# Kernel optimization log

Hardware: AMD Instinct MI355X
Metric: run time of the kernel (lower is better)

## Reference

```python
import jax, jax.numpy as jnp
import numpy as np

N_NODES = 50000
N_EDGES = 600000
IN_FEATS = 128
N_HIDDEN = 128
N_CLASSES = 64


def setup_inputs() -> dict:
    key = jax.random.key(0)
    ks = jax.random.split(key, 10)
    x = jax.random.normal(ks[0], (N_NODES, IN_FEATS), dtype=jnp.float32)
    w = jax.random.uniform(ks[1], (N_EDGES,), dtype=jnp.float32)
    src = jax.random.randint(ks[2], (N_EDGES,), 0, N_NODES, dtype=jnp.int32)
    dst = jax.random.randint(ks[3], (N_EDGES,), 0, N_NODES, dtype=jnp.int32)
    W1 = jax.random.normal(ks[4], (IN_FEATS, N_HIDDEN), dtype=jnp.float32) * 0.05
    b1 = jnp.zeros((N_HIDDEN,), dtype=jnp.float32)
    W2 = jax.random.normal(ks[5], (N_HIDDEN, N_HIDDEN), dtype=jnp.float32) * 0.05
    b2 = jnp.zeros((N_HIDDEN,), dtype=jnp.float32)
    W3 = jax.random.normal(ks[6], (N_HIDDEN, N_CLASSES), dtype=jnp.float32) * 0.05
    b3 = jnp.zeros((N_CLASSES,), dtype=jnp.float32)
    return {"x": x, "w": w, "src": src, "dst": dst,
            "W1": W1, "b1": b1, "W2": W2, "b2": b2, "W3": W3, "b3": b3}


def _graph_conv(h, Wl, bl, w, src, dst, n_nodes):
    # dense linear transform
    h = h @ Wl + bl  # [N, d_out]
    # u_mul_e: gather source features, scale by edge weight
    m = h[src] * w[:, None]  # [E, d_out]
    # sum aggregation into destination nodes
    return jax.ops.segment_sum(m, dst, num_segments=n_nodes)  # [N, d_out]


def reference(x, w, src, dst, W1, b1, W2, b2, W3, b3):
    n = x.shape[0]
    h = jax.nn.relu(_graph_conv(x, W1, b1, w, src, dst, n))
    h = jax.nn.relu(_graph_conv(h, W2, b2, w, src, dst, n))
    return _graph_conv(h, W3, b3, w, src, dst, n)
```

## Files before the change

kernel.cpp:

```cpp
#include <hip/hip_runtime.h>
#include <hip/hip_fp16.h>


typedef __attribute__((ext_vector_type(8))) short short8;
typedef __attribute__((ext_vector_type(4))) float float4v;

constexpr int CAP  = 48;
constexpr int CPAD = 16;

__device__ inline unsigned bf16_rne(float f) {
    unsigned u = __float_as_uint(f);
    return (u + 0x7FFF + ((u >> 16) & 1)) >> 16;
}
__device__ inline float bf_lo(unsigned t) { return __uint_as_float(t << 16); }
__device__ inline float bf_hi(unsigned t) { return __uint_as_float(t & 0xFFFF0000u); }

__device__ inline unsigned pack_rec(int s, float wv) {
    return ((unsigned)__half_as_ushort(__float2half(wv)) << 16) | (unsigned)s;
}
__device__ inline float rec_w(unsigned r) {
    return __half2float(__ushort_as_half((unsigned short)(r >> 16)));
}
__device__ inline int rec_src(unsigned r) { return (int)(r & 0xFFFFu); }

__device__ inline void wprep_one(const float* __restrict__ Wm, int M, int tt,
                                 unsigned short* __restrict__ WfH,
                                 unsigned short* __restrict__ WfL) {
    const int FT = M / 16;
    int lane = tt & 63;
    int ft   = (tt >> 6) % FT;
    int ks   = tt / (64 * FT);
    int n     = ft * 16 + (lane & 15);
    int kbase = ks * 32 + (lane >> 4) * 8;
    #pragma unroll
    for (int j = 0; j < 8; j++) {
        float wv = Wm[(size_t)(kbase + j) * M + n];
        unsigned hb = bf16_rne(wv);
        float wh = __uint_as_float(hb << 16);
        unsigned lb = bf16_rne(wv - wh);
        WfH[(size_t)tt * 8 + j] = (unsigned short)hb;
        WfL[(size_t)tt * 8 + j] = (unsigned short)lb;
    }
}

__global__ void prep_kernel(const float* __restrict__ W1, const float* __restrict__ W2,
                            const float* __restrict__ W3,
                            unsigned short* WfH1, unsigned short* WfL1,
                            unsigned short* WfH2, unsigned short* WfL2,
                            unsigned short* WfH3, unsigned short* WfL3,
                            int* __restrict__ countsP, int N) {
    int t = blockIdx.x * blockDim.x + threadIdx.x;
    if (t < 2048)       wprep_one(W1, 128, t,        WfH1, WfL1);
    else if (t < 4096)  wprep_one(W2, 128, t - 2048, WfH2, WfL2);
    else if (t < 5120)  wprep_one(W3,  64, t - 4096, WfH3, WfL3);
    for (int i = t; i < N; i += gridDim.x * blockDim.x) countsP[i * CPAD] = 0;
}

__global__ __launch_bounds__(256) void l1_fused(
        const float* __restrict__ H,
        const unsigned short* __restrict__ WfH, const unsigned short* __restrict__ WfL,
        const float* __restrict__ bias, unsigned short* __restrict__ T,
        const int* __restrict__ src, const int* __restrict__ dst,
        const float* __restrict__ w, int* __restrict__ countsP,
        unsigned* __restrict__ erec, int N, int E, int SB) {
    const int K  = 128;
    const int KP = K + 4;
    const int M  = 128;
    const int FT = M / 16;
    __shared__ float Hs[64 * KP];

    if ((int)blockIdx.x < SB) {
        int e = (blockIdx.x * 256 + threadIdx.x) * 4;
        if (e + 3 < E) {
            int4   d4 = *(const int4*)(dst + e);
            int4   s4 = *(const int4*)(src + e);
            float4 w4 = *(const float4*)(w + e);
            unsigned r0 = pack_rec(s4.x, w4.x);
            unsigned r1 = pack_rec(s4.y, w4.y);
            unsigned r2 = pack_rec(s4.z, w4.z);
            unsigned r3 = pack_rec(s4.w, w4.w);
            int p0 = atomicAdd(&countsP[d4.x * CPAD], 1);
            int p1 = atomicAdd(&countsP[d4.y * CPAD], 1);
            int p2 = atomicAdd(&countsP[d4.z * CPAD], 1);
            int p3 = atomicAdd(&countsP[d4.w * CPAD], 1);
            if (p0 < CAP) erec[(size_t)d4.x * CAP + p0] = r0;
            if (p1 < CAP) erec[(size_t)d4.y * CAP + p1] = r1;
            if (p2 < CAP) erec[(size_t)d4.z * CAP + p2] = r2;
            if (p3 < CAP) erec[(size_t)d4.w * CAP + p3] = r3;
        } else {
            for (; e < E; e++) {
                int d = dst[e];
                unsigned r = pack_rec(src[e], w[e]);
                int p = atomicAdd(&countsP[d * CPAD], 1);
                if (p < CAP) erec[(size_t)d * CAP + p] = r;
            }
        }
        return;
    }

    const int node0 = (blockIdx.x - SB) * 64;
    for (int i = threadIdx.x; i < 64 * (K / 4); i += 256) {
        int r = i / (K / 4), c = i % (K / 4);
        int node = node0 + r;
        float4 hv = {0, 0, 0, 0};
        if (node < N) hv = ((const float4*)(H + (size_t)node * K))[c];
        *(float4*)(Hs + r * KP + c * 4) = hv;
    }
    __syncthreads();

    const int wave = threadIdx.x >> 6;
    const int lane = threadIdx.x & 63;
    const int row  = lane & 15;
    const int ksub = (lane >> 4) * 8;
    const float* hrow = Hs + (wave * 16 + row) * KP;

    float4v acc[FT];
    #pragma unroll
    for (int ft = 0; ft < FT; ft++) acc[ft] = (float4v){0.f, 0.f, 0.f, 0.f};

    #pragma unroll
    for (int ks = 0; ks < 4; ks++) {
        const float* ap = hrow + ks * 32 + ksub;
        float4 a0 = *(const float4*)(ap);
        float4 a1 = *(const float4*)(ap + 4);
        float av[8] = {a0.x, a0.y, a0.z, a0.w, a1.x, a1.y, a1.z, a1.w};
        short8 ah, al;
        #pragma unroll
        for (int j = 0; j < 8; j++) {
            unsigned hb = bf16_rne(av[j]);
            float fh = __uint_as_float(hb << 16);
            ah[j] = (short)hb;
            al[j] = (short)bf16_rne(av[j] - fh);
        }
        #pragma unroll
        for (int ft = 0; ft < FT; ft++) {
            short8 bh = *(const short8*)(WfH + ((size_t)(ks * FT + ft) * 64 + lane) * 8);
            short8 bl = *(const short8*)(WfL + ((size_t)(ks * FT + ft) * 64 + lane) * 8);
            acc[ft] = __builtin_amdgcn_mfma_f32_16x16x32_bf16(ah, bh, acc[ft], 0, 0, 0);
            acc[ft] = __builtin_amdgcn_mfma_f32_16x16x32_bf16(al, bh, acc[ft], 0, 0, 0);
            acc[ft] = __builtin_amdgcn_mfma_f32_16x16x32_bf16(ah, bl, acc[ft], 0, 0, 0);
        }
    }

    const int col   = lane & 15;
    const int rbase = (lane >> 4) * 4;
    #pragma unroll
    for (int ft = 0; ft < FT; ft++) {
        int feat = ft * 16 + col;
        float bv = bias[feat];
        #pragma unroll
        for (int r = 0; r < 4; r++) {
            int node = node0 + wave * 16 + rbase + r;
            if (node < N)
                T[(size_t)node * M + feat] = (unsigned short)bf16_rne(acc[ft][r] + bv);
        }
    }
}

template <int M>
__global__ __launch_bounds__(256) void gemm_bf_kernel(const unsigned short* __restrict__ Hb,
                                                      const unsigned short* __restrict__ WfH,
                                                      const unsigned short* __restrict__ WfL,
                                                      const float* __restrict__ bias,
                                                      unsigned short* __restrict__ T, int N) {
    const int FT = M / 16;
    const int wave = threadIdx.x >> 6;
    const int lane = threadIdx.x & 63;
    const int row  = lane & 15;
    const int ksub = (lane >> 4) * 8;
    const int node0 = blockIdx.x * 64;
    int nodeA = node0 + wave * 16 + row;
    const unsigned short* hp = Hb + (size_t)(nodeA < N ? nodeA : N - 1) * 128;

    float4v acc[FT];
    #pragma unroll
    for (int ft = 0; ft < FT; ft++) acc[ft] = (float4v){0.f, 0.f, 0.f, 0.f};

    #pragma unroll
    for (int ks = 0; ks < 4; ks++) {
        short8 ah = *(const short8*)(hp + ks * 32 + ksub);
        #pragma unroll
        for (int ft = 0; ft < FT; ft++) {
            short8 bh = *(const short8*)(WfH + ((size_t)(ks * FT + ft) * 64 + lane) * 8);
            short8 bl = *(const short8*)(WfL + ((size_t)(ks * FT + ft) * 64 + lane) * 8);
            acc[ft] = __builtin_amdgcn_mfma_f32_16x16x32_bf16(ah, bh, acc[ft], 0, 0, 0);
            acc[ft] = __builtin_amdgcn_mfma_f32_16x16x32_bf16(ah, bl, acc[ft], 0, 0, 0);
        }
    }

    const int col   = lane & 15;
    const int rbase = (lane >> 4) * 4;
    #pragma unroll
    for (int ft = 0; ft < FT; ft++) {
        int feat = ft * 16 + col;
        float bv = bias[feat];
        #pragma unroll
        for (int r = 0; r < 4; r++) {
            int node = node0 + wave * 16 + rbase + r;
            if (node < N)
                T[(size_t)node * M + feat] = (unsigned short)bf16_rne(acc[ft][r] + bv);
        }
    }
}

__global__ void agg128_bf(const unsigned short* __restrict__ Tin,
                          const int* __restrict__ countsP,
                          const unsigned* __restrict__ erec,
                          unsigned short* __restrict__ Hb, int N) {
    const int wid  = threadIdx.x >> 6;
    const int lane = threadIdx.x & 63;
    const int v0 = blockIdx.x * 8 + wid * 2;
    if (v0 >= N) return;
    const int v1 = (v0 + 1 < N) ? v0 + 1 : v0;
    const int q  = lane >> 4;
    const int fo = (lane & 15) * 8;
    const unsigned* eb0 = erec + (size_t)v0 * CAP;
    const unsigned* eb1 = erec + (size_t)v1 * CAP;

    int rx0[4], rx1[4]; float wv0[4], wv1[4];
    #pragma unroll
    for (int u = 0; u < 4; u++) {
        unsigned r0 = eb0[u * 4 + q];
        unsigned r1 = eb1[u * 4 + q];
        rx0[u] = rec_src(r0); wv0[u] = rec_w(r0);
        rx1[u] = rec_src(r1); wv1[u] = rec_w(r1);
    }
    const int c0 = min(countsP[v0 * CPAD], CAP);
    const int c1 = min(countsP[v1 * CPAD], CAP);
    const int cm = max(c0, c1);

    float A0[8] = {0, 0, 0, 0, 0, 0, 0, 0};
    float A1[8] = {0, 0, 0, 0, 0, 0, 0, 0};
    for (int i = 0; i < cm; i += 16) {
        #pragma unroll
        for (int u = 0; u < 4; u++) {
            int idx = i + u * 4 + q;
            if (idx < c0) {
                uint4 t = *(const uint4*)(Tin + (size_t)rx0[u] * 128 + fo);
                float wu = wv0[u];
                A0[0] = fmaf(wu, bf_lo(t.x), A0[0]); A0[1] = fmaf(wu, bf_hi(t.x), A0[1]);
                A0[2] = fmaf(wu, bf_lo(t.y), A0[2]); A0[3] = fmaf(wu, bf_hi(t.y), A0[3]);
                A0[4] = fmaf(wu, bf_lo(t.z), A0[4]); A0[5] = fmaf(wu, bf_hi(t.z), A0[5]);
                A0[6] = fmaf(wu, bf_lo(t.w), A0[6]); A0[7] = fmaf(wu, bf_hi(t.w), A0[7]);
            }
            if (idx < c1) {
                uint4 t = *(const uint4*)(Tin + (size_t)rx1[u] * 128 + fo);
                float wu = wv1[u];
                A1[0] = fmaf(wu, bf_lo(t.x), A1[0]); A1[1] = fmaf(wu, bf_hi(t.x), A1[1]);
                A1[2] = fmaf(wu, bf_lo(t.y), A1[2]); A1[3] = fmaf(wu, bf_hi(t.y), A1[3]);
                A1[4] = fmaf(wu, bf_lo(t.z), A1[4]); A1[5] = fmaf(wu, bf_hi(t.z), A1[5]);
                A1[6] = fmaf(wu, bf_lo(t.w), A1[6]); A1[7] = fmaf(wu, bf_hi(t.w), A1[7]);
            }
        }
        if (i + 16 < cm) {
            #pragma unroll
            for (int u = 0; u < 4; u++) {
                unsigned r0 = eb0[i + 16 + u * 4 + q];
                unsigned r1 = eb1[i + 16 + u * 4 + q];
                rx0[u] = rec_src(r0); wv0[u] = rec_w(r0);
                rx1[u] = rec_src(r1); wv1[u] = rec_w(r1);
            }
        }
    }
    #pragma unroll
    for (int j = 0; j < 8; j++) {
        A0[j] += __shfl_xor(A0[j], 32); A1[j] += __shfl_xor(A1[j], 32);
        A0[j] += __shfl_xor(A0[j], 16); A1[j] += __shfl_xor(A1[j], 16);
    }
    if (lane < 16) {
        short8 o;
        #pragma unroll
        for (int j = 0; j < 8; j++) o[j] = (short)bf16_rne(fmaxf(A0[j], 0.f));
        *(short8*)(Hb + (size_t)v0 * 128 + fo) = o;
    } else if (lane < 32 && v1 != v0) {
        short8 o;
        #pragma unroll
        for (int j = 0; j < 8; j++) o[j] = (short)bf16_rne(fmaxf(A1[j], 0.f));
        *(short8*)(Hb + (size_t)v1 * 128 + fo) = o;
    }
}

__global__ void agg_final_v4(const unsigned short* __restrict__ Tin,
                             const int* __restrict__ countsP,
                             const unsigned* __restrict__ erec,
                             float* __restrict__ OUT, int N) {
    const int wid  = threadIdx.x >> 6;
    const int lane = threadIdx.x & 63;
    const int v0 = blockIdx.x * 8 + wid * 2;
    if (v0 >= N) return;
    const int v1 = (v0 + 1 < N) ? v0 + 1 : v0;
    const int o8 = lane >> 3;
    const int fo = (lane & 7) * 8;
    const unsigned* eb0 = erec + (size_t)v0 * CAP;
    const unsigned* eb1 = erec + (size_t)v1 * CAP;

    int rx0[2], rx1[2]; float wv0[2], wv1[2];
    #pragma unroll
    for (int u = 0; u < 2; u++) {
        unsigned r0 = eb0[u * 8 + o8];
        unsigned r1 = eb1[u * 8 + o8];
        rx0[u] = rec_src(r0); wv0[u] = rec_w(r0);
        rx1[u] = rec_src(r1); wv1[u] = rec_w(r1);
    }
    const int c0 = min(countsP[v0 * CPAD], CAP);
    const int c1 = min(countsP[v1 * CPAD], CAP);
    const int cm = max(c0, c1);

    float A0[8] = {0, 0, 0, 0, 0, 0, 0, 0};
    float A1[8] = {0, 0, 0, 0, 0, 0, 0, 0};
    for (int i = 0; i < cm; i += 16) {
        #pragma unroll
        for (int u = 0; u < 2; u++) {
            int idx = i + u * 8 + o8;
            if (idx < c0) {
                uint4 t = *(const uint4*)(Tin + (size_t)rx0[u] * 64 + fo);
                float wu = wv0[u];
                A0[0] = fmaf(wu, bf_lo(t.x), A0[0]); A0[1] = fmaf(wu, bf_hi(t.x), A0[1]);
                A0[2] = fmaf(wu, bf_lo(t.y), A0[2]); A0[3] = fmaf(wu, bf_hi(t.y), A0[3]);
                A0[4] = fmaf(wu, bf_lo(t.z), A0[4]); A0[5] = fmaf(wu, bf_hi(t.z), A0[5]);
                A0[6] = fmaf(wu, bf_lo(t.w), A0[6]); A0[7] = fmaf(wu, bf_hi(t.w), A0[7]);
            }
            if (idx < c1) {
                uint4 t = *(const uint4*)(Tin + (size_t)rx1[u] * 64 + fo);
                float wu = wv1[u];
                A1[0] = fmaf(wu, bf_lo(t.x), A1[0]); A1[1] = fmaf(wu, bf_hi(t.x), A1[1]);
                A1[2] = fmaf(wu, bf_lo(t.y), A1[2]); A1[3] = fmaf(wu, bf_hi(t.y), A1[3]);
                A1[4] = fmaf(wu, bf_lo(t.z), A1[4]); A1[5] = fmaf(wu, bf_hi(t.z), A1[5]);
                A1[6] = fmaf(wu, bf_lo(t.w), A1[6]); A1[7] = fmaf(wu, bf_hi(t.w), A1[7]);
            }
        }
        if (i + 16 < cm) {
            #pragma unroll
            for (int u = 0; u < 2; u++) {
                unsigned r0 = eb0[i + 16 + u * 8 + o8];
                unsigned r1 = eb1[i + 16 + u * 8 + o8];
                rx0[u] = rec_src(r0); wv0[u] = rec_w(r0);
                rx1[u] = rec_src(r1); wv1[u] = rec_w(r1);
            }
        }
    }
    #pragma unroll
    for (int j = 0; j < 8; j++) {
        A0[j] += __shfl_xor(A0[j], 32); A1[j] += __shfl_xor(A1[j], 32);
        A0[j] += __shfl_xor(A0[j], 16); A1[j] += __shfl_xor(A1[j], 16);
        A0[j] += __shfl_xor(A0[j], 8);  A1[j] += __shfl_xor(A1[j], 8);
    }
    if (lane < 8) {
        float4 o0 = {A0[0], A0[1], A0[2], A0[3]};
        float4 o1 = {A0[4], A0[5], A0[6], A0[7]};
        float* op = OUT + (size_t)v0 * 64 + fo;
        *(float4*)(op)     = o0;
        *(float4*)(op + 4) = o1;
    } else if (lane < 16 && v1 != v0) {
        float4 o0 = {A1[0], A1[1], A1[2], A1[3]};
        float4 o1 = {A1[4], A1[5], A1[6], A1[7]};
        float* op = OUT + (size_t)v1 * 64 + fo;
        *(float4*)(op)     = o0;
        *(float4*)(op + 4) = o1;
    }
}

extern "C" void kernel_launch(void* const* d_in, const int* in_sizes, int n_in,
                              void* d_out, int out_size, void* d_ws, size_t ws_size,
                              hipStream_t stream) {
    const float* x   = (const float*)d_in[0];
    const float* w   = (const float*)d_in[1];
    const int*   src = (const int*)d_in[2];
    const int*   dst = (const int*)d_in[3];
    const float* W1  = (const float*)d_in[4];
    const float* b1  = (const float*)d_in[5];
    const float* W2  = (const float*)d_in[6];
    const float* b2  = (const float*)d_in[7];
    const float* W3  = (const float*)d_in[8];
    const float* b3  = (const float*)d_in[9];
    const int N = in_sizes[0] / 128;
    const int E = in_sizes[1];

    unsigned short* Tbf  = (unsigned short*)d_ws;
    unsigned short* Hbf  = Tbf + (size_t)N * 128;
    unsigned* erec = (unsigned*)(Hbf + (size_t)N * 128);
    int*  countsP  = (int*)(erec + (size_t)N * CAP);
    size_t coff = (size_t)((char*)(countsP + (size_t)N * CPAD) - (char*)d_ws);
    coff = (coff + 15) & ~(size_t)15;
    unsigned short* WfH1 = (unsigned short*)((char*)d_ws + coff);
    unsigned short* WfL1 = WfH1 + 128 * 128;
    unsigned short* WfH2 = WfL1 + 128 * 128;
    unsigned short* WfL2 = WfH2 + 128 * 128;
    unsigned short* WfH3 = WfL2 + 128 * 128;
    unsigned short* WfL3 = WfH3 + 128 * 64;

    const int GB = (N + 63) / 64;
    const int SB = (E / 4 + 255) / 256;
    const int AB = (N + 7) / 8;

    prep_kernel<<<96, 256, 0, stream>>>(W1, W2, W3, WfH1, WfL1, WfH2, WfL2,
                                        WfH3, WfL3, countsP, N);
    l1_fused<<<SB + GB, 256, 0, stream>>>(x, WfH1, WfL1, b1, Tbf,
                                          src, dst, w, countsP, erec, N, E, SB);
    agg128_bf<<<AB, 256, 0, stream>>>(Tbf, countsP, erec, Hbf, N);
    gemm_bf_kernel<128><<<GB, 256, 0, stream>>>(Hbf, WfH2, WfL2, b2, Tbf, N);
    agg128_bf<<<AB, 256, 0, stream>>>(Tbf, countsP, erec, Hbf, N);
    gemm_bf_kernel<64><<<GB, 256, 0, stream>>>(Hbf, WfH3, WfL3, b3, Tbf, N);
    agg_final_v4<<<AB, 256, 0, stream>>>(Tbf, countsP, erec, (float*)d_out, N);
}
```

Before: 240.7 us.

## Fuse neighbor aggregation with next-layer GEMM through shared memory

Merges each aggregation kernel with the following dense transform. A 512-thread block aggregates 16 nodes into shared memory, then each wave computes one 16-column output tile with MFMA. This removes the intermediate H round trip through global memory and two kernel launches, and ping-pongs between two T buffers. It also shrinks the layer-1 GEMM tile to 32 nodes per block with column-split waves to get more blocks. The cost is lower MFMA reuse per block and a block-wide barrier between the gather and GEMM phases; in the 64-column layer half the waves sit idle during the GEMM.

```diff
diff --git a/kernel.cpp b/kernel.cpp
--- a/kernel.cpp
+++ b/kernel.cpp
@@ -65,9 +65,7 @@
         unsigned* __restrict__ erec, int N, int E, int SB) {
     const int K  = 128;
     const int KP = K + 4;
-    const int M  = 128;
-    const int FT = M / 16;
-    __shared__ float Hs[64 * KP];
+    __shared__ float Hs[32 * KP];
 
     if ((int)blockIdx.x < SB) {
         int e = (blockIdx.x * 256 + threadIdx.x) * 4;
@@ -98,9 +96,9 @@
         return;
     }
 
-    const int node0 = (blockIdx.x - SB) * 64;
-    for (int i = threadIdx.x; i < 64 * (K / 4); i += 256) {
-        int r = i / (K / 4), c = i % (K / 4);
+    const int node0 = (blockIdx.x - SB) * 32;
+    for (int i = threadIdx.x; i < 32 * (K / 4); i += 256) {
+        int r = i >> 5, c = i & 31;
         int node = node0 + r;
         float4 hv = {0, 0, 0, 0};
         if (node < N) hv = ((const float4*)(H + (size_t)node * K))[c];
@@ -112,11 +110,13 @@
     const int lane = threadIdx.x & 63;
     const int row  = lane & 15;
     const int ksub = (lane >> 4) * 8;
-    const float* hrow = Hs + (wave * 16 + row) * KP;
-
-    float4v acc[FT];
-    #pragma unroll
-    for (int ft = 0; ft < FT; ft++) acc[ft] = (float4v){0.f, 0.f, 0.f, 0.f};
+    const int rbase16 = (wave >> 1) * 16;
+    const int ftbase  = (wave & 1) * 4;
+    const float* hrow = Hs + (rbase16 + row) * KP;
+
+    float4v acc[4];
+    #pragma unroll
+    for (int ft = 0; ft < 4; ft++) acc[ft] = (float4v){0.f, 0.f, 0.f, 0.f};
 
     #pragma unroll
     for (int ks = 0; ks < 4; ks++) {
@@ -133,9 +133,10 @@
             al[j] = (short)bf16_rne(av[j] - fh);
         }
         #pragma unroll
-        for (int ft = 0; ft < FT; ft++) {
-            short8 bh = *(const short8*)(WfH + ((size_t)(ks * FT + ft) * 64 + lane) * 8);
-            short8 bl = *(const short8*)(WfL + ((size_t)(ks * FT + ft) * 64 + lane) * 8);
+        for (int ft = 0; ft < 4; ft++) {
+            int ftg = ftbase + ft;
+            short8 bh = *(const short8*)(WfH + ((size_t)(ks * 8 + ftg) * 64 + lane) * 8);
+            short8 bl = *(const short8*)(WfL + ((size_t)(ks * 8 + ftg) * 64 + lane) * 8);
             acc[ft] = __builtin_amdgcn_mfma_f32_16x16x32_bf16(ah, bh, acc[ft], 0, 0, 0);
             acc[ft] = __builtin_amdgcn_mfma_f32_16x16x32_bf16(al, bh, acc[ft], 0, 0, 0);
             acc[ft] = __builtin_amdgcn_mfma_f32_16x16x32_bf16(ah, bl, acc[ft], 0, 0, 0);
@@ -145,77 +146,38 @@
     const int col   = lane & 15;
     const int rbase = (lane >> 4) * 4;
     #pragma unroll
-    for (int ft = 0; ft < FT; ft++) {
-        int feat = ft * 16 + col;
+    for (int ft = 0; ft < 4; ft++) {
+        int feat = (ftbase + ft) * 16 + col;
         float bv = bias[feat];
         #pragma unroll
         for (int r = 0; r < 4; r++) {
-            int node = node0 + wave * 16 + rbase + r;
+            int node = node0 + rbase16 + rbase + r;
             if (node < N)
-                T[(size_t)node * M + feat] = (unsigned short)bf16_rne(acc[ft][r] + bv);
-        }
-    }
-}
-
-template <int M>
-__global__ __launch_bounds__(256) void gemm_bf_kernel(const unsigned short* __restrict__ Hb,
-                                                      const unsigned short* __restrict__ WfH,
-                                                      const unsigned short* __restrict__ WfL,
-                                                      const float* __restrict__ bias,
-                                                      unsigned short* __restrict__ T, int N) {
-    const int FT = M / 16;
-    const int wave = threadIdx.x >> 6;
-    const int lane = threadIdx.x & 63;
-    const int row  = lane & 15;
-    const int ksub = (lane >> 4) * 8;
-    const int node0 = blockIdx.x * 64;
-    int nodeA = node0 + wave * 16 + row;
-    const unsigned short* hp = Hb + (size_t)(nodeA < N ? nodeA : N - 1) * 128;
-
-    float4v acc[FT];
-    #pragma unroll
-    for (int ft = 0; ft < FT; ft++) acc[ft] = (float4v){0.f, 0.f, 0.f, 0.f};
-
-    #pragma unroll
-    for (int ks = 0; ks < 4; ks++) {
-        short8 ah = *(const short8*)(hp + ks * 32 + ksub);
-        #pragma unroll
-        for (int ft = 0; ft < FT; ft++) {
-            short8 bh = *(const short8*)(WfH + ((size_t)(ks * FT + ft) * 64 + lane) * 8);
-            short8 bl = *(const short8*)(WfL + ((size_t)(ks * FT + ft) * 64 + lane) * 8);
-            acc[ft] = __builtin_amdgcn_mfma_f32_16x16x32_bf16(ah, bh, acc[ft], 0, 0, 0);
-            acc[ft] = __builtin_amdgcn_mfma_f32_16x16x32_bf16(ah, bl, acc[ft], 0, 0, 0);
-        }
-    }
-
-    const int col   = lane & 15;
-    const int rbase = (lane >> 4) * 4;
-    #pragma unroll
-    for (int ft = 0; ft < FT; ft++) {
-        int feat = ft * 16 + col;
-        float bv = bias[feat];
-        #pragma unroll
-        for (int r = 0; r < 4; r++) {
-            int node = node0 + wave * 16 + rbase + r;
-            if (node < N)
-                T[(size_t)node * M + feat] = (unsigned short)bf16_rne(acc[ft][r] + bv);
-        }
-    }
-}
-
-__global__ void agg128_bf(const unsigned short* __restrict__ Tin,
-                          const int* __restrict__ countsP,
-                          const unsigned* __restrict__ erec,
-                          unsigned short* __restrict__ Hb, int N) {
+                T[(size_t)node * 128 + feat] = (unsigned short)bf16_rne(acc[ft][r] + bv);
+        }
+    }
+}
+
+template <int MOUT>
+__global__ __launch_bounds__(512) void agg_gemm(
+        const unsigned short* __restrict__ Tin,
+        const int* __restrict__ countsP,
+        const unsigned* __restrict__ erec,
+        const unsigned short* __restrict__ WfH, const unsigned short* __restrict__ WfL,
+        const float* __restrict__ bias,
+        unsigned short* __restrict__ T, int N) {
+    constexpr int FT = MOUT / 16;
     const int wid  = threadIdx.x >> 6;
     const int lane = threadIdx.x & 63;
-    const int v0 = blockIdx.x * 8 + wid * 2;
-    if (v0 >= N) return;
-    const int v1 = (v0 + 1 < N) ? v0 + 1 : v0;
+    __shared__ unsigned short Hsm[16][136];
+
+    int v0 = blockIdx.x * 16 + wid * 2;
+    int v0c = (v0 < N) ? v0 : N - 1;
+    int v1c = (v0 + 1 < N) ? v0 + 1 : N - 1;
     const int q  = lane >> 4;
     const int fo = (lane & 15) * 8;
-    const unsigned* eb0 = erec + (size_t)v0 * CAP;
-    const unsigned* eb1 = erec + (size_t)v1 * CAP;
+    const unsigned* eb0 = erec + (size_t)v0c * CAP;
+    const unsigned* eb1 = erec + (size_t)v1c * CAP;
 
     int rx0[4], rx1[4]; float wv0[4], wv1[4];
     #pragma unroll
@@ -225,8 +187,8 @@
         rx0[u] = rec_src(r0); wv0[u] = rec_w(r0);
         rx1[u] = rec_src(r1); wv1[u] = rec_w(r1);
     }
-    const int c0 = min(countsP[v0 * CPAD], CAP);
-    const int c1 = min(countsP[v1 * CPAD], CAP);
+    const int c0 = min(countsP[v0c * CPAD], CAP);
+    const int c1 = min(countsP[v1c * CPAD], CAP);
     const int cm = max(c0, c1);
 
     float A0[8] = {0, 0, 0, 0, 0, 0, 0, 0};
@@ -271,12 +233,38 @@
         short8 o;
         #pragma unroll
         for (int j = 0; j < 8; j++) o[j] = (short)bf16_rne(fmaxf(A0[j], 0.f));
-        *(short8*)(Hb + (size_t)v0 * 128 + fo) = o;
-    } else if (lane < 32 && v1 != v0) {
+        *(short8*)&Hsm[wid * 2][lane * 8] = o;
+    } else if (lane < 32) {
         short8 o;
         #pragma unroll
         for (int j = 0; j < 8; j++) o[j] = (short)bf16_rne(fmaxf(A1[j], 0.f));
-        *(short8*)(Hb + (size_t)v1 * 128 + fo) = o;
+        *(short8*)&Hsm[wid * 2 + 1][(lane & 15) * 8] = o;
+    }
+    __syncthreads();
+
+    if (FT == 8 || wid < FT) {
+        const int ftg  = wid;
+        const int row  = lane & 15;
+        const int ksub = (lane >> 4) * 8;
+        float4v acc = (float4v){0.f, 0.f, 0.f, 0.f};
+        #pragma unroll
+        for (int ks = 0; ks < 4; ks++) {
+            short8 ah = *(const short8*)&Hsm[row][ks * 32 + ksub];
+            short8 bh = *(const short8*)(WfH + ((size_t)(ks * FT + ftg) * 64 + lane) * 8);
+            short8 bl = *(const short8*)(WfL + ((size_t)(ks * FT + ftg) * 64 + lane) * 8);
+            acc = __builtin_amdgcn_mfma_f32_16x16x32_bf16(ah, bh, acc, 0, 0, 0);
+            acc = __builtin_amdgcn_mfma_f32_16x16x32_bf16(ah, bl, acc, 0, 0, 0);
+        }
+        const int col   = lane & 15;
+        const int rbase = (lane >> 4) * 4;
+        const int feat  = ftg * 16 + col;
+        const float bv  = bias[feat];
+        #pragma unroll
+        for (int r = 0; r < 4; r++) {
+            int node = blockIdx.x * 16 + rbase + r;
+            if (node < N)
+                T[(size_t)node * MOUT + feat] = (unsigned short)bf16_rne(acc[r] + bv);
+        }
     }
 }
 
@@ -376,9 +364,9 @@
     const int N = in_sizes[0] / 128;
     const int E = in_sizes[1];
 
-    unsigned short* Tbf  = (unsigned short*)d_ws;
-    unsigned short* Hbf  = Tbf + (size_t)N * 128;
-    unsigned* erec = (unsigned*)(Hbf + (size_t)N * 128);
+    unsigned short* Ta   = (unsigned short*)d_ws;
+    unsigned short* Tb   = Ta + (size_t)N * 128;
+    unsigned* erec = (unsigned*)(Tb + (size_t)N * 128);
     int*  countsP  = (int*)(erec + (size_t)N * CAP);
     size_t coff = (size_t)((char*)(countsP + (size_t)N * CPAD) - (char*)d_ws);
     coff = (coff + 15) & ~(size_t)15;
@@ -389,17 +377,16 @@
     unsigned short* WfH3 = WfL2 + 128 * 128;
     unsigned short* WfL3 = WfH3 + 128 * 64;
 
-    const int GB = (N + 63) / 64;
-    const int SB = (E / 4 + 255) / 256;
-    const int AB = (N + 7) / 8;
+    const int GB  = (N + 31) / 32;
+    const int SB  = (E / 4 + 255) / 256;
+    const int AGB = (N + 15) / 16;
+    const int AB  = (N + 7) / 8;
 
     prep_kernel<<<96, 256, 0, stream>>>(W1, W2, W3, WfH1, WfL1, WfH2, WfL2,
                                         WfH3, WfL3, countsP, N);
-    l1_fused<<<SB + GB, 256, 0, stream>>>(x, WfH1, WfL1, b1, Tbf,
+    l1_fused<<<SB + GB, 256, 0, stream>>>(x, WfH1, WfL1, b1, Ta,
                                           src, dst, w, countsP, erec, N, E, SB);
-    agg128_bf<<<AB, 256, 0, stream>>>(Tbf, countsP, erec, Hbf, N);
-    gemm_bf_kernel<128><<<GB, 256, 0, stream>>>(Hbf, WfH2, WfL2, b2, Tbf, N);
-    agg128_bf<<<AB, 256, 0, stream>>>(Tbf, countsP, erec, Hbf, N);
-    gemm_bf_kernel<64><<<GB, 256, 0, stream>>>(Hbf, WfH3, WfL3, b3, Tbf, N);
-    agg_final_v4<<<AB, 256, 0, stream>>>(Tbf, countsP, erec, (float*)d_out, N);
-}
+    agg_gemm<128><<<AGB, 512, 0, stream>>>(Ta, countsP, erec, WfH2, WfL2, b2, Tb, N);
+    agg_gemm<64><<<AGB, 512, 0, stream>>>(Tb, countsP, erec, WfH3, WfL3, b3, Ta, N);
+    agg_final_v4<<<AB, 256, 0, stream>>>(Ta, countsP, erec, (float*)d_out, N);
+}
```

Measured after the change: 215.1 us, median of 2. -10.6%, faster.
